# Performance work log

Hardware: AMD Instinct MI355X
Metric: run time of the kernel (lower is better)

The kernel has to match this reference:

```python
import jax, jax.numpy as jnp
import numpy as np

DIM = 1024
B, K = 8192, 16


def setup_inputs() -> dict:
    key = jax.random.key(0)
    ks = jax.random.split(key, 7)
    # xavier_uniform bound for square [C,C]: sqrt(6/(C+C))
    bq = float(np.sqrt(6.0 / (DIM + DIM)))
    ba_bound = float(np.sqrt(6.0 / (DIM + 1)))
    return {
        "query": jax.random.normal(ks[0], (B, DIM), dtype=jnp.float32),
        "key": jax.random.normal(ks[1], (B, K, DIM), dtype=jnp.float32),
        "value": jax.random.normal(ks[2], (B, K, DIM), dtype=jnp.float32),
        "Wq": jax.random.uniform(ks[3], (DIM, DIM), jnp.float32, -bq, bq),
        "Wk": jax.random.uniform(ks[4], (DIM, DIM), jnp.float32, -bq, bq),
        "Wa": jax.random.uniform(ks[5], (1, DIM), jnp.float32, -ba_bound, ba_bound),
        "ba": jnp.ones((1,), dtype=jnp.float32),
    }


def reference(query, key, value, Wq, Wk, Wa, ba):
    # query: [B, C]; key/value: [B, K, C]
    C = query.shape[-1]
    res = query
    q = query[:, None, :]                       # [B, 1, C]
    k = jnp.concatenate([q, key], axis=1)       # [B, K+1, C] (query prepended)
    v = jnp.concatenate([q, value], axis=1)     # [B, K+1, C]
    qp = q @ Wq.T                               # [B, 1, C]
    kp = k @ Wk.T                               # [B, K+1, C]
    scale = 1.0 / jnp.sqrt(jnp.asarray(C, dtype=jnp.float32))
    scores = jnp.einsum('bqc,bkc->bqk', qp, kp) * scale   # [B, 1, K+1]
    attn_w = jax.nn.softmax(scores, axis=-1)
    attn = jnp.einsum('bqk,bkc->bqc', attn_w, v)[:, 0, :]  # [B, C]
    alpha = jax.nn.sigmoid(res @ Wa.T + ba)     # [B, 1]
    out = res + alpha * attn                    # gated residual
    # F.normalize(p=2, dim=-1, eps=1e-12)
    norm = jnp.linalg.norm(out, axis=-1, keepdims=True)
    return out / jnp.maximum(norm, 1e-12)
```

## Files before the change

kernel.cpp:

```cpp
#include <hip/hip_runtime.h>
#include <hip/hip_bf16.h>

#define DIM   1024
#define BATCH 8192
#define KV    16

typedef __attribute__((ext_vector_type(4))) float f32x4;
typedef __attribute__((ext_vector_type(8))) short short8;

static __device__ __forceinline__ unsigned short f2bf(float x) {
  return __builtin_bit_cast(unsigned short, __float2bfloat16(x));
}
static __device__ __forceinline__ float bf2f(unsigned short x) {
  return __bfloat162float(__builtin_bit_cast(__hip_bfloat16, x));
}
static __device__ __forceinline__ float dot4(f32x4 a, f32x4 b) {
  return a.x * b.x + a.y * b.y + a.z * b.z + a.w * b.w;
}

static __device__ __forceinline__ void gl_lds16(const unsigned short* g, unsigned short* l) {
  __builtin_amdgcn_global_load_lds(
      (const __attribute__((address_space(1))) void*)g,
      (__attribute__((address_space(3))) void*)l, 16, 0, 0);
}

__global__ __launch_bounds__(256) void transpose_w(const float* __restrict__ Wq,
                                                   const float* __restrict__ Wk,
                                                   unsigned short* __restrict__ WqT,
                                                   unsigned short* __restrict__ WkT) {
  __shared__ float tile[32][33];
  const float* src = blockIdx.z ? Wk : Wq;
  unsigned short* dst = blockIdx.z ? WkT : WqT;
  int tx = threadIdx.x & 31, ty = threadIdx.x >> 5;
  int x = blockIdx.x * 32 + tx;
  int y0 = blockIdx.y * 32;
  #pragma unroll
  for (int i = ty; i < 32; i += 8)
    tile[i][tx] = src[(size_t)(y0 + i) * DIM + x];
  __syncthreads();
  int x2 = blockIdx.y * 32 + tx;
  int y2 = blockIdx.x * 32;
  #pragma unroll
  for (int i = ty; i < 32; i += 8)
    dst[(size_t)(y2 + i) * DIM + x2] = f2bf(tile[tx][i]);
}

__global__ __launch_bounds__(512) void gemm_nt64ks(const unsigned short* __restrict__ A,
                                                   const unsigned short* __restrict__ B,
                                                   unsigned short* __restrict__ C,
                                                   int N, int K) {
  __shared__ __align__(16) unsigned short As[2][64 * 32];
  __shared__ __align__(16) unsigned short Bs[2][64 * 32];
  __shared__ float Cred[64 * 65];
  const int tid = threadIdx.x;
  const int half = tid >> 8;
  const int htid = tid & 255;
  const int lane = tid & 63;
  const int wave4 = (tid >> 6) & 3;
  const int wr = wave4 >> 1, wc = wave4 & 1;
  const size_t bm = (size_t)blockIdx.x * 64;
  const size_t bn = (size_t)blockIdx.y * 64;

  f32x4 acc[2][2];
  #pragma unroll
  for (int m = 0; m < 2; ++m)
    #pragma unroll
    for (int n = 0; n < 2; ++n)
      acc[m][n] = (f32x4){0.f, 0.f, 0.f, 0.f};

  const int r0 = htid >> 2;
  const int cc = (htid & 3) * 8;
  const int kg = lane >> 4;
  const int rowf = lane & 15;
  const int kbase = half * (K / 2);

  for (int k32 = 0; k32 < K / 64; ++k32) {
    const int kt = kbase + k32 * 32;
    gl_lds16(A + (bm + r0) * K + kt + cc, As[half] + htid * 8);
    gl_lds16(B + (bn + r0) * K + kt + cc, Bs[half] + htid * 8);
    __syncthreads();
    short8 af[2], bfr[2];
    #pragma unroll
    for (int m = 0; m < 2; ++m)
      af[m] = *(const short8*)(As[half] + ((wr * 32 + m * 16 + rowf) * 32 + kg * 8));
    #pragma unroll
    for (int n = 0; n < 2; ++n)
      bfr[n] = *(const short8*)(Bs[half] + ((wc * 32 + n * 16 + rowf) * 32 + kg * 8));
    #pragma unroll
    for (int m = 0; m < 2; ++m)
      #pragma unroll
      for (int n = 0; n < 2; ++n)
        acc[m][n] = __builtin_amdgcn_mfma_f32_16x16x32_bf16(af[m], bfr[n], acc[m][n], 0, 0, 0);
    __syncthreads();
  }

  const int rq = (lane >> 4) * 4;
  const int colf = lane & 15;
  if (half == 1) {
    #pragma unroll
    for (int m = 0; m < 2; ++m)
      #pragma unroll
      for (int n = 0; n < 2; ++n)
        #pragma unroll
        for (int i = 0; i < 4; ++i)
          Cred[(wr * 32 + m * 16 + rq + i) * 65 + wc * 32 + n * 16 + colf] = acc[m][n][i];
  }
  __syncthreads();
  if (half == 0) {
    #pragma unroll
    for (int m = 0; m < 2; ++m)
      #pragma unroll
      for (int n = 0; n < 2; ++n)
        #pragma unroll
        for (int i = 0; i < 4; ++i) {
          int row = wr * 32 + m * 16 + rq + i;
          int col = wc * 32 + n * 16 + colf;
          float v = acc[m][n][i] + Cred[row * 65 + col];
          C[(bm + row) * N + bn + col] = f2bf(v);
        }
  }
}

__global__ __launch_bounds__(512) void gemm_u(const float* __restrict__ Af,
                                              const unsigned short* __restrict__ B,
                                              unsigned short* __restrict__ C,
                                              int ntN, int ldc) {
  __shared__ __align__(16) unsigned short As[128 * 32];
  __shared__ __align__(16) unsigned short Bs[128 * 32];

  const int cpx = gridDim.x >> 3;
  const int wg = (blockIdx.x & 7) * cpx + (blockIdx.x >> 3);
  const size_t bm = (size_t)(wg / ntN) * 128;
  const size_t bn = (size_t)(wg % ntN) * 128;

  const int tid = threadIdx.x;
  const int lane = tid & 63;
  const int wave = tid >> 6;
  const int wr = wave >> 2, wc = wave & 3;

  f32x4 acc[4][2];
  #pragma unroll
  for (int m = 0; m < 4; ++m)
    #pragma unroll
    for (int n = 0; n < 2; ++n)
      acc[m][n] = (f32x4){0.f, 0.f, 0.f, 0.f};

  const int kg = lane >> 4;
  const int rowf = lane & 15;
  const int br0 = tid >> 2;
  const int bcc = (tid & 3) * 8;
  const int ar0 = tid >> 3;
  const int ak = (tid & 7) * 4;

  f32x4 pref[2];
  pref[0] = *(const f32x4*)(Af + (bm + ar0) * DIM + ak);
  pref[1] = *(const f32x4*)(Af + (bm + 64 + ar0) * DIM + ak);

  for (int kt = 0; kt < DIM; kt += 32) {
    gl_lds16(B + (bn + br0) * DIM + kt + bcc, Bs + tid * 8);
    {
      ushort4 o0, o1;
      o0.x = f2bf(pref[0].x); o0.y = f2bf(pref[0].y);
      o0.z = f2bf(pref[0].z); o0.w = f2bf(pref[0].w);
      o1.x = f2bf(pref[1].x); o1.y = f2bf(pref[1].y);
      o1.z = f2bf(pref[1].z); o1.w = f2bf(pref[1].w);
      *(ushort4*)(As + ar0 * 32 + ak) = o0;
      *(ushort4*)(As + (64 + ar0) * 32 + ak) = o1;
    }
    __syncthreads();
    if (kt + 32 < DIM) {
      pref[0] = *(const f32x4*)(Af + (bm + ar0) * DIM + kt + 32 + ak);
      pref[1] = *(const f32x4*)(Af + (bm + 64 + ar0) * DIM + kt + 32 + ak);
    }
    short8 af[4], bfr[2];
    #pragma unroll
    for (int m = 0; m < 4; ++m)
      af[m] = *(const short8*)(As + ((wr * 64 + m * 16 + rowf) * 32 + kg * 8));
    #pragma unroll
    for (int n = 0; n < 2; ++n)
      bfr[n] = *(const short8*)(Bs + ((wc * 32 + n * 16 + rowf) * 32 + kg * 8));
    #pragma unroll
    for (int m = 0; m < 4; ++m)
      #pragma unroll
      for (int n = 0; n < 2; ++n)
        acc[m][n] = __builtin_amdgcn_mfma_f32_16x16x32_bf16(af[m], bfr[n], acc[m][n], 0, 0, 0);
    __syncthreads();
  }

  const int rq = (lane >> 4) * 4;
  const int colf = lane & 15;
  #pragma unroll
  for (int m = 0; m < 4; ++m)
    #pragma unroll
    for (int n = 0; n < 2; ++n)
      #pragma unroll
      for (int i = 0; i < 4; ++i) {
        size_t row = bm + wr * 64 + m * 16 + rq + i;
        size_t col = bn + wc * 32 + n * 16 + colf;
        C[row * (size_t)ldc + col] = f2bf(acc[m][n][i]);
      }
}

__global__ __launch_bounds__(256) void epilogue(const float* __restrict__ query,
                                                const float* __restrict__ key,
                                                const float* __restrict__ value,
                                                const float* __restrict__ Wa,
                                                const float* __restrict__ ba,
                                                const unsigned short* __restrict__ u,
                                                float* __restrict__ out) {
  const int b = blockIdx.x;
  const int tid = threadIdx.x;
  const int lane = tid & 63, wave = tid >> 6;
  const f32x4* k4 = (const f32x4*)(key + (size_t)b * KV * DIM);
  const f32x4* v4 = (const f32x4*)(value + (size_t)b * KV * DIM);

  f32x4 qv = ((const f32x4*)(query + (size_t)b * DIM))[tid];
  ushort4 ub = ((const ushort4*)(u + (size_t)b * 2048))[tid];
  f32x4 uv;
  uv.x = bf2f(ub.x); uv.y = bf2f(ub.y); uv.z = bf2f(ub.z); uv.w = bf2f(ub.w);
  f32x4 wv = ((const f32x4*)Wa)[tid];

  float s[17];
  s[0] = dot4(qv, uv);
  float ad = dot4(qv, wv);
  #pragma unroll
  for (int j = 1; j <= 16; ++j) {
    f32x4 kv = __builtin_nontemporal_load(k4 + (j - 1) * 256 + tid);
    s[j] = dot4(uv, kv);
  }

  f32x4 vv[16];
  #pragma unroll
  for (int j = 0; j < 16; ++j)
    vv[j] = __builtin_nontemporal_load(v4 + j * 256 + tid);

  #pragma unroll
  for (int m = 32; m >= 1; m >>= 1) {
    #pragma unroll
    for (int j = 0; j < 17; ++j) s[j] += __shfl_xor(s[j], m);
    ad += __shfl_xor(ad, m);
  }
  __shared__ float red[4][18];
  if (lane == 0) {
    #pragma unroll
    for (int j = 0; j < 17; ++j) red[wave][j] = s[j];
    red[wave][17] = ad;
  }
  __syncthreads();

  float wt[17];
  float mx = -1e30f;
  #pragma unroll
  for (int j = 0; j < 17; ++j) {
    float t = (red[0][j] + red[1][j] + red[2][j] + red[3][j]) * 0.03125f;
    wt[j] = t;
    mx = fmaxf(mx, t);
  }
  float den = 0.f;
  #pragma unroll
  for (int j = 0; j < 17; ++j) {
    wt[j] = expf(wt[j] - mx);
    den += wt[j];
  }
  float adt = red[0][17] + red[1][17] + red[2][17] + red[3][17] + ba[0];
  float alpha = 1.0f / (1.0f + expf(-adt));
  float am = alpha / den;

  f32x4 acc = qv * wt[0];
  #pragma unroll
  for (int j = 1; j <= 16; ++j) acc += vv[j - 1] * wt[j];
  f32x4 t = qv + acc * am;

  float ssp = dot4(t, t);
  #pragma unroll
  for (int m = 32; m >= 1; m >>= 1) ssp += __shfl_xor(ssp, m);
  __shared__ float red2[4];
  if (lane == 0) red2[wave] = ssp;
  __syncthreads();
  float nrm = sqrtf(red2[0] + red2[1] + red2[2] + red2[3]);
  float inv = 1.0f / fmaxf(nrm, 1e-12f);

  __builtin_nontemporal_store(t * inv, (f32x4*)(out + (size_t)b * DIM) + tid);
}

extern "C" void kernel_launch(void* const* d_in, const int* in_sizes, int n_in,
                              void* d_out, int out_size, void* d_ws, size_t ws_size,
                              hipStream_t stream) {
  const float* query = (const float*)d_in[0];
  const float* key   = (const float*)d_in[1];
  const float* value = (const float*)d_in[2];
  const float* Wq    = (const float*)d_in[3];
  const float* Wk    = (const float*)d_in[4];
  const float* Wa    = (const float*)d_in[5];
  const float* ba    = (const float*)d_in[6];

  unsigned short* WqT = (unsigned short*)d_ws;
  unsigned short* WkT = WqT + (size_t)DIM * DIM;
  unsigned short* Mt  = WkT + (size_t)DIM * DIM;
  unsigned short* ubf = (unsigned short*)d_out;

  transpose_w<<<dim3(32, 32, 2), 256, 0, stream>>>(Wq, Wk, WqT, WkT);
  gemm_nt64ks<<<dim3(16, 16), 512, 0, stream>>>(WkT, WqT, Mt, DIM, DIM);
  gemm_u<<<512, 512, 0, stream>>>(query, Mt, ubf, DIM / 128, 2048);
  epilogue<<<BATCH, 256, 0, stream>>>(query, key, value, Wa, ba, ubf, (float*)d_out);
}
```

Measured before the change: 235.8 us.

## Split query GEMM K-dimension across two block halves with LDS reduction

The u = query·M GEMM now uses 128x64 output tiles and 1024 blocks, and each block's two 256-thread halves each cover half of the K range. Partial accumulators are summed through shared memory before the bf16 store. The goal is more parallelism and a shorter serial K loop per block, to hide load latency. In exchange, each block loads the fp32 query tile twice as often relative to its output and adds a reduction step and an extra sync.

```diff
diff --git a/kernel.cpp b/kernel.cpp
--- a/kernel.cpp
+++ b/kernel.cpp
@@ -121,22 +121,26 @@
   }
 }
 
-__global__ __launch_bounds__(512) void gemm_u(const float* __restrict__ Af,
-                                              const unsigned short* __restrict__ B,
-                                              unsigned short* __restrict__ C,
-                                              int ntN, int ldc) {
-  __shared__ __align__(16) unsigned short As[128 * 32];
-  __shared__ __align__(16) unsigned short Bs[128 * 32];
+__global__ __launch_bounds__(512) void gemm_u_ks(const float* __restrict__ Af,
+                                                 const unsigned short* __restrict__ B,
+                                                 unsigned short* __restrict__ C,
+                                                 int ntN, int ldc) {
+  __shared__ __align__(16) char smem[128 * 65 * 4];
+  unsigned short* Ash = (unsigned short*)(smem + (threadIdx.x >> 8) * 8192);
+  unsigned short* Bsh = (unsigned short*)(smem + 16384 + (threadIdx.x >> 8) * 4096);
+  float* Cred = (float*)smem;
 
   const int cpx = gridDim.x >> 3;
   const int wg = (blockIdx.x & 7) * cpx + (blockIdx.x >> 3);
   const size_t bm = (size_t)(wg / ntN) * 128;
-  const size_t bn = (size_t)(wg % ntN) * 128;
+  const size_t bn = (size_t)(wg % ntN) * 64;
 
   const int tid = threadIdx.x;
+  const int half = tid >> 8;
+  const int htid = tid & 255;
   const int lane = tid & 63;
-  const int wave = tid >> 6;
-  const int wr = wave >> 2, wc = wave & 3;
+  const int wave4 = (tid >> 6) & 3;
+  const int wr = wave4 >> 1, wc = wave4 & 1;
 
   f32x4 acc[4][2];
   #pragma unroll
@@ -147,38 +151,43 @@
 
   const int kg = lane >> 4;
   const int rowf = lane & 15;
-  const int br0 = tid >> 2;
-  const int bcc = (tid & 3) * 8;
-  const int ar0 = tid >> 3;
-  const int ak = (tid & 7) * 4;
-
-  f32x4 pref[2];
-  pref[0] = *(const f32x4*)(Af + (bm + ar0) * DIM + ak);
-  pref[1] = *(const f32x4*)(Af + (bm + 64 + ar0) * DIM + ak);
-
-  for (int kt = 0; kt < DIM; kt += 32) {
-    gl_lds16(B + (bn + br0) * DIM + kt + bcc, Bs + tid * 8);
-    {
-      ushort4 o0, o1;
-      o0.x = f2bf(pref[0].x); o0.y = f2bf(pref[0].y);
-      o0.z = f2bf(pref[0].z); o0.w = f2bf(pref[0].w);
-      o1.x = f2bf(pref[1].x); o1.y = f2bf(pref[1].y);
-      o1.z = f2bf(pref[1].z); o1.w = f2bf(pref[1].w);
-      *(ushort4*)(As + ar0 * 32 + ak) = o0;
-      *(ushort4*)(As + (64 + ar0) * 32 + ak) = o1;
+  const int br0 = htid >> 2;
+  const int bcc = (htid & 3) * 8;
+  const int kbase = half * 512;
+
+  f32x4 pref[4];
+  #pragma unroll
+  for (int it = 0; it < 4; ++it) {
+    int c = it * 256 + htid;
+    pref[it] = *(const f32x4*)(Af + (bm + (c >> 3)) * DIM + kbase + (c & 7) * 4);
+  }
+
+  for (int k32 = 0; k32 < 16; ++k32) {
+    const int kt = kbase + k32 * 32;
+    gl_lds16(B + (bn + br0) * DIM + kt + bcc, Bsh + htid * 8);
+    #pragma unroll
+    for (int it = 0; it < 4; ++it) {
+      int c = it * 256 + htid;
+      ushort4 o;
+      o.x = f2bf(pref[it].x); o.y = f2bf(pref[it].y);
+      o.z = f2bf(pref[it].z); o.w = f2bf(pref[it].w);
+      *(ushort4*)(Ash + c * 4) = o;
     }
     __syncthreads();
-    if (kt + 32 < DIM) {
-      pref[0] = *(const f32x4*)(Af + (bm + ar0) * DIM + kt + 32 + ak);
-      pref[1] = *(const f32x4*)(Af + (bm + 64 + ar0) * DIM + kt + 32 + ak);
+    if (k32 + 1 < 16) {
+      #pragma unroll
+      for (int it = 0; it < 4; ++it) {
+        int c = it * 256 + htid;
+        pref[it] = *(const f32x4*)(Af + (bm + (c >> 3)) * DIM + kt + 32 + (c & 7) * 4);
+      }
     }
     short8 af[4], bfr[2];
     #pragma unroll
     for (int m = 0; m < 4; ++m)
-      af[m] = *(const short8*)(As + ((wr * 64 + m * 16 + rowf) * 32 + kg * 8));
+      af[m] = *(const short8*)(Ash + ((wr * 64 + m * 16 + rowf) * 32 + kg * 8));
     #pragma unroll
     for (int n = 0; n < 2; ++n)
-      bfr[n] = *(const short8*)(Bs + ((wc * 32 + n * 16 + rowf) * 32 + kg * 8));
+      bfr[n] = *(const short8*)(Bsh + ((wc * 32 + n * 16 + rowf) * 32 + kg * 8));
     #pragma unroll
     for (int m = 0; m < 4; ++m)
       #pragma unroll
@@ -189,16 +198,29 @@
 
   const int rq = (lane >> 4) * 4;
   const int colf = lane & 15;
-  #pragma unroll
-  for (int m = 0; m < 4; ++m)
-    #pragma unroll
-    for (int n = 0; n < 2; ++n)
-      #pragma unroll
-      for (int i = 0; i < 4; ++i) {
-        size_t row = bm + wr * 64 + m * 16 + rq + i;
-        size_t col = bn + wc * 32 + n * 16 + colf;
-        C[row * (size_t)ldc + col] = f2bf(acc[m][n][i]);
-      }
+  if (half == 1) {
+    #pragma unroll
+    for (int m = 0; m < 4; ++m)
+      #pragma unroll
+      for (int n = 0; n < 2; ++n)
+        #pragma unroll
+        for (int i = 0; i < 4; ++i)
+          Cred[(wr * 64 + m * 16 + rq + i) * 65 + wc * 32 + n * 16 + colf] = acc[m][n][i];
+  }
+  __syncthreads();
+  if (half == 0) {
+    #pragma unroll
+    for (int m = 0; m < 4; ++m)
+      #pragma unroll
+      for (int n = 0; n < 2; ++n)
+        #pragma unroll
+        for (int i = 0; i < 4; ++i) {
+          int row = wr * 64 + m * 16 + rq + i;
+          int col = wc * 32 + n * 16 + colf;
+          float v = acc[m][n][i] + Cred[row * 65 + col];
+          C[(bm + row) * (size_t)ldc + bn + col] = f2bf(v);
+        }
+  }
 }
 
 __global__ __launch_bounds__(256) void epilogue(const float* __restrict__ query,
@@ -301,6 +323,6 @@
 
   transpose_w<<<dim3(32, 32, 2), 256, 0, stream>>>(Wq, Wk, WqT, WkT);
   gemm_nt64ks<<<dim3(16, 16), 512, 0, stream>>>(WkT, WqT, Mt, DIM, DIM);
-  gemm_u<<<512, 512, 0, stream>>>(query, Mt, ubf, DIM / 128, 2048);
+  gemm_u_ks<<<1024, 512, 0, stream>>>(query, Mt, ubf, DIM / 64, 2048);
   epilogue<<<BATCH, 256, 0, stream>>>(query, key, value, Wa, ba, ubf, (float*)d_out);
 }
```

Result: slower. 243.7 us (+3.4%).
